# Optimization experiments

Measured on AMD Instinct MI355X. Metric: run time of the kernel, lower is better.

The kernel has to match this reference:

```python
import jax, jax.numpy as jnp
import numpy as np

N = 32; D = 1152; HEADS = 16; HD = D // HEADS; DEPTH = 12
C = 4; GS = 16; P = GS * GS; PL = 16; FE = 256; NC = 1000; MLPD = 4 * D
L = C + P; SCALE = HD ** -0.5


def _ln(x, g, b):
    m = x.mean(-1, keepdims=True)
    v = ((x - m) ** 2).mean(-1, keepdims=True)
    return (x - m) * jax.lax.rsqrt(v + 1e-5) * g + b


def _sincos_pos_embed(dim, gs):
    def _1d(ed, pos):
        omega = 1.0 / 10000 ** (np.arange(ed // 2, dtype=np.float64) / (ed / 2.0))
        out = np.einsum('m,d->md', pos.reshape(-1), omega)
        return np.concatenate([np.sin(out), np.cos(out)], axis=1)
    gw, gh = np.meshgrid(np.arange(gs, dtype=np.float32), np.arange(gs, dtype=np.float32))
    return np.concatenate([_1d(dim // 2, gw), _1d(dim // 2, gh)], axis=1)


def setup_inputs():
    key = jax.random.key(0)
    ks = iter(jax.random.split(key, 64))
    r = lambda *s: 0.02 * jax.random.normal(next(ks), s, dtype=jnp.float32)
    inp = {}
    inp['x'] = jax.random.normal(next(ks), (N, P, PL), dtype=jnp.float32)
    inp['t'] = jax.random.uniform(next(ks), (N,), dtype=jnp.float32) * 1000.0
    inp['y'] = jax.random.randint(next(ks), (N,), 0, NC)
    inp['xw'] = r(PL, D); inp['xb'] = r(D)
    inp['tw1'] = r(FE, D); inp['tb1'] = r(D)
    inp['tw2'] = r(D, D); inp['tb2'] = r(D)
    inp['ytab'] = r(NC + 1, D * C)
    inp['pos'] = jnp.asarray(_sincos_pos_embed(D, GS)[None], dtype=jnp.float32)
    inp['cpos'] = r(1, C, D)
    inp['ln1g'] = 1.0 + r(DEPTH, D); inp['ln1b'] = r(DEPTH, D)
    inp['qkvw'] = r(DEPTH, D, 3 * D)
    inp['qng'] = 1.0 + r(DEPTH, HD); inp['qnb'] = r(DEPTH, HD)
    inp['kng'] = 1.0 + r(DEPTH, HD); inp['knb'] = r(DEPTH, HD)
    inp['pw'] = r(DEPTH, D, D); inp['pb'] = r(DEPTH, D)
    inp['ln2g'] = 1.0 + r(DEPTH, D); inp['ln2b'] = r(DEPTH, D)
    inp['f1w'] = r(DEPTH, D, MLPD); inp['f1b'] = r(DEPTH, MLPD)
    inp['f2w'] = r(DEPTH, MLPD, D); inp['f2b'] = r(DEPTH, D)
    inp['fng'] = 1.0 + r(D); inp['fnb'] = r(D)
    inp['ow'] = r(D, PL); inp['ob'] = r(PL)
    return inp


def reference(x, t, y, xw, xb, tw1, tb1, tw2, tb2, ytab, pos, cpos,
              ln1g, ln1b, qkvw, qng, qnb, kng, knb, pw, pb,
              ln2g, ln2b, f1w, f1b, f2w, f2b, fng, fnb, ow, ob):
    n = x.shape[0]
    # timestep embedding (sinusoidal -> MLP with SiLU)
    half = FE // 2
    freqs = jnp.exp(-jnp.log(jnp.float32(10000.0)) * jnp.arange(half, dtype=jnp.float32) / half)
    a = t[:, None] * freqs[None]
    temb = jnp.concatenate([jnp.cos(a), jnp.sin(a)], axis=-1)  # [N, FE]
    temb = jax.nn.silu(temb @ tw1 + tb1) @ tw2 + tb2           # [N, D]
    # label embedding -> num_cond_tokens conditioning tokens (eval: no label drop)
    cond = ytab[y].reshape(n, C, D) + cpos + temb[:, None, :]  # [N, C, D]
    # patch token projection + fixed sincos pos embed
    xt = x @ xw + xb + pos                                     # [N, P, D]
    tok = jnp.concatenate([cond, xt], axis=1)                  # [N, L, D]
    mask = jnp.triu(jnp.ones((L, L), dtype=bool), k=1)         # causal (True = masked)

    def block(tok, p):
        g1, b1, qw, qg, qb, kg, kb, pww, pbb, g2, b2, w1, bb1, w2, bb2 = p
        h = _ln(tok, g1, b1)
        qkv = (h @ qw).reshape(n, L, 3, HEADS, HD).transpose(2, 0, 3, 1, 4)
        q, k, v = qkv[0], qkv[1], qkv[2]                       # [N, H, L, HD]
        q = _ln(q, qg, qb) * SCALE
        k = _ln(k, kg, kb)
        att = jnp.einsum('nhqd,nhkd->nhqk', q, k)
        att = jnp.where(mask, jnp.float32(-1e9), att)
        att = jax.nn.softmax(att, axis=-1)
        o = jnp.einsum('nhqk,nhkd->nhqd', att, v).transpose(0, 2, 1, 3).reshape(n, L, D)
        tok = tok + (o @ pww + pbb)
        h2 = _ln(tok, g2, b2)
        tok = tok + (jax.nn.gelu(h2 @ w1 + bb1, approximate=True) @ w2 + bb2)
        return tok, None

    tok, _ = jax.lax.scan(block, tok,
                          (ln1g, ln1b, qkvw, qng, qnb, kng, knb, pw, pb,
                           ln2g, ln2b, f1w, f1b, f2w, f2b))
    out = _ln(tok, fng, fnb) @ ow + ob                          # [N, L, PL]
    return out[:, C:]                                           # predictions for patch tokens
```

## Files before the change

kernel.cpp:

```cpp
#include <hip/hip_runtime.h>
#include <hip/hip_bf16.h>
#include <cstdint>

#define DEV __device__ __forceinline__

typedef __attribute__((ext_vector_type(8))) short bf16x8;
typedef __attribute__((ext_vector_type(4))) float f32x4;
typedef unsigned short u16;
typedef unsigned int u32;

constexpr int BN_   = 32;
constexpr int PP    = 256;
constexpr int PL_   = 16;
constexpr int CT    = 4;
constexpr int LL    = 260;
constexpr int DD    = 1152;
constexpr int HH    = 16;
constexpr int HDIM  = 72;
constexpr int DEPTH_= 12;
constexpr int TD    = 3456;
constexpr int MLPD_ = 4608;
constexpr int MREAL = BN_*LL;
constexpr int MPAD  = 8448;
constexpr int LP    = 288;
constexpr int HDP   = 96;
constexpr int HDV   = 80;
constexpr float SCALE_ = 0.11785113019775793f;

constexpr size_t OP_ = (size_t)TD*DD;
constexpr size_t OF1 = OP_ + (size_t)DD*DD;
constexpr size_t OF2 = OF1 + (size_t)MLPD_*DD;
constexpr size_t ARENA_ELEMS = OF2 + (size_t)1280*MLPD_;

DEV u16 f2bf(float f){
    union{float f; u32 i;} c; c.f = f;
    u32 u = c.i;
    u32 r = (u + 0x7fffu + ((u>>16)&1u)) >> 16;
    return (u16)r;
}
DEV float bf2f(u32 u){ union{u32 i; float f;} c; c.i = u<<16; return c.f; }

DEV float wave_sum64(float v){
    #pragma unroll
    for (int off=32; off; off>>=1) v += __shfl_xor(v, off);
    return v;
}
DEV float group16_sum(float v){
    #pragma unroll
    for (int off=8; off; off>>=1) v += __shfl_xor(v, off);
    return v;
}
DEV float gelu_f(float x){
    float u = 0.7978845608028654f * (x + 0.044715f * x*x*x);
    return x / (1.f + __expf(-2.f * u));
}

__global__ void temb1_kernel(const float* __restrict__ t, const float* __restrict__ tw1,
                             const float* __restrict__ tb1, float* __restrict__ e1)
{
    int n = blockIdx.y, j = blockIdx.x*128 + threadIdx.x;
    float tv = t[n];
    float acc = tb1[j];
    const float k = 0.07195578415606394f;
    for (int i = 0; i < 128; ++i) {
        float f = __expf(-k * (float)i);
        float a = tv * f;
        float sa = sinf(a), ca = cosf(a);
        acc += ca * tw1[(size_t)i*DD + j] + sa * tw1[(size_t)(i+128)*DD + j];
    }
    e1[(size_t)n*DD + j] = acc / (1.f + __expf(-acc));
}

__global__ void temb2_kernel(const float* __restrict__ e1, const float* __restrict__ tw2,
                             const float* __restrict__ tb2, float* __restrict__ te)
{
    int n = blockIdx.y, j = blockIdx.x*128 + threadIdx.x;
    float acc = tb2[j];
    const float* er = e1 + (size_t)n*DD;
    for (int kk = 0; kk < DD; ++kk)
        acc += er[kk] * tw2[(size_t)kk*DD + j];
    te[(size_t)n*DD + j] = acc;
}

__global__ void assemble_kernel(const float* __restrict__ x, const int* __restrict__ y,
                                const float* __restrict__ xw, const float* __restrict__ xb,
                                const float* __restrict__ ytab, const float* __restrict__ pos,
                                const float* __restrict__ cpos, const float* __restrict__ te,
                                float* __restrict__ tokf)
{
    int m = blockIdx.x;
    if (m >= MREAL) {
        for (int d = threadIdx.x; d < DD; d += 256) tokf[(size_t)m*DD + d] = 0.f;
        return;
    }
    int n = m / LL, l = m % LL;
    if (l < CT) {
        int cls = y[n];
        const float* yt = ytab + (size_t)cls*(CT*DD) + (size_t)l*DD;
        const float* cp = cpos + (size_t)l*DD;
        const float* tm = te + (size_t)n*DD;
        for (int d = threadIdx.x; d < DD; d += 256)
            tokf[(size_t)m*DD + d] = yt[d] + cp[d] + tm[d];
    } else {
        int p = l - CT;
        const float* xr = x + (size_t)(n*PP + p)*PL_;
        float xv[16];
        #pragma unroll
        for (int i=0;i<16;i++) xv[i] = xr[i];
        const float* pr = pos + (size_t)p*DD;
        for (int d = threadIdx.x; d < DD; d += 256) {
            float acc = xb[d] + pr[d];
            #pragma unroll
            for (int i=0;i<16;i++) acc += xv[i] * xw[(size_t)i*DD + d];
            tokf[(size_t)m*DD + d] = acc;
        }
    }
}

__global__ void convT4_kernel(const float* __restrict__ qkvw, const float* __restrict__ pw,
                              const float* __restrict__ f1w, const float* __restrict__ f2w,
                              u16* __restrict__ arena)
{
    __shared__ float tile[64][65];
    int id = blockIdx.x;
    const float* W; u16* WT; int K, Nw, t0;
    if (id < 972)        { W = qkvw; WT = arena;        K = DD;    Nw = TD;    t0 = id; }
    else if (id < 1296)  { W = pw;   WT = arena + OP_;  K = DD;    Nw = DD;    t0 = id - 972; }
    else if (id < 2592)  { W = f1w;  WT = arena + OF1;  K = DD;    Nw = MLPD_; t0 = id - 1296; }
    else                 { W = f2w;  WT = arena + OF2;  K = MLPD_; Nw = DD;    t0 = id - 2592; }
    int nx = Nw >> 6;
    int nb = (t0 % nx) * 64, kb = (t0 / nx) * 64;
    int tx = threadIdx.x & 63, ty = threadIdx.x >> 6;
    #pragma unroll
    for (int r=0;r<16;r++)
        tile[r*4 + ty][tx] = W[(size_t)(kb + r*4 + ty)*Nw + nb + tx];
    __syncthreads();
    int j = threadIdx.x & 63, i2 = threadIdx.x >> 6;
    #pragma unroll
    for (int r=0;r<16;r++) {
        int n = i2 + r*4;
        WT[(size_t)(nb + n)*K + kb + j] = f2bf(tile[j][n]);
    }
}

__global__ void ln_kernel(const float* __restrict__ src, const float* __restrict__ g,
                          const float* __restrict__ b, u16* __restrict__ dst)
{
    int lane = threadIdx.x & 63, w = threadIdx.x >> 6;
    int m = blockIdx.x*4 + w;
    const float* row = src + (size_t)m * DD;
    float4 v[5];
    float s = 0.f, ss = 0.f;
    #pragma unroll
    for (int i=0;i<5;i++) {
        int idx = i*64 + lane;
        if (idx < 288) {
            v[i] = ((const float4*)row)[idx];
            s  += v[i].x + v[i].y + v[i].z + v[i].w;
            ss += v[i].x*v[i].x + v[i].y*v[i].y + v[i].z*v[i].z + v[i].w*v[i].w;
        }
    }
    s = wave_sum64(s); ss = wave_sum64(ss);
    float mean = s * (1.f/DD);
    float var  = ss * (1.f/DD) - mean*mean;
    float rs   = rsqrtf(var + 1e-5f);
    u16* orow = dst + (size_t)m*DD;
    #pragma unroll
    for (int i=0;i<5;i++) {
        int idx = i*64 + lane;
        if (idx < 288) {
            int c0 = idx*4;
            float4 gg = ((const float4*)g)[idx];
            float4 bb = ((const float4*)b)[idx];
            ushort4 o;
            o.x = f2bf((v[i].x-mean)*rs*gg.x + bb.x);
            o.y = f2bf((v[i].y-mean)*rs*gg.y + bb.y);
            o.z = f2bf((v[i].z-mean)*rs*gg.z + bb.z);
            o.w = f2bf((v[i].w-mean)*rs*gg.w + bb.w);
            *(ushort4*)(orow + c0) = o;
        }
    }
}

template<int EPI>
__global__ __launch_bounds__(256, 4)
void gemm97_kernel(const u16* __restrict__ A, const u16* __restrict__ BT,
                   int K, int Nreal, u16* __restrict__ outb, float* __restrict__ outf,
                   const float* __restrict__ bias)
{
    __shared__ u16 As[128][64];
    __shared__ u16 Bs[128][64];
    const int tid = threadIdx.x;
    const int lane = tid & 63, wv = tid >> 6;
    const int wq = wv >> 1, wp = wv & 1;
    const int l15 = lane & 15, g4 = lane >> 4;

    const int id = blockIdx.x + gridDim.x * blockIdx.y;
    const int total = gridDim.x * gridDim.y;
    const int qch = total >> 3, rch = total & 7;
    const int xcd = id & 7, ps = id >> 3;
    const int wg = (xcd < rch ? xcd*(qch+1) : rch*(qch+1) + (xcd-rch)*qch) + ps;
    const int m0 = (wg / gridDim.x) * 128, n0 = (wg % gridDim.x) * 128;

    const int rr = tid >> 3, chv = tid & 7;
    const int cxo = (chv ^ (rr & 7)) * 8;
    const u16* gA = A  + (size_t)(m0 + rr) * K + cxo;
    const u16* gB = BT + (size_t)(n0 + rr) * K + cxo;

    auto stageA = [&](int kk) {
        #pragma unroll
        for (int i=0;i<4;i++)
            __builtin_amdgcn_global_load_lds(
                (const __attribute__((address_space(1))) void*)(gA + (size_t)(i*32)*K + kk),
                (__attribute__((address_space(3))) void*)(&As[i*32 + wv*8][0]), 16, 0, 0);
    };
    auto stageB = [&](int kk) {
        #pragma unroll
        for (int i=0;i<4;i++)
            __builtin_amdgcn_global_load_lds(
                (const __attribute__((address_space(1))) void*)(gB + (size_t)(i*32)*K + kk),
                (__attribute__((address_space(3))) void*)(&Bs[i*32 + wv*8][0]), 16, 0, 0);
    };
    auto rdA = [&](int m, int ks)->bf16x8 {
        int r = wq*64 + m*16 + l15;
        return *(const bf16x8*)(&As[r][((ks*4 + g4) ^ (r & 7))*8]);
    };
    auto rdB = [&](int n, int ks)->bf16x8 {
        int r = wp*64 + n*16 + l15;
        return *(const bf16x8*)(&Bs[r][((ks*4 + g4) ^ (r & 7))*8]);
    };

    f32x4 acc[4][4];
    #pragma unroll
    for (int i=0;i<4;i++)
        #pragma unroll
        for (int j=0;j<4;j++) acc[i][j] = (f32x4){0.f,0.f,0.f,0.f};

    const int NT = K >> 6;
    for (int t = 0; t < NT; ++t) {
        stageA(t << 6); stageB(t << 6);
        __syncthreads();
        #pragma unroll
        for (int ks=0; ks<2; ++ks) {
            bf16x8 aF[4], bF[4];
            #pragma unroll
            for (int m=0;m<4;m++) aF[m] = rdA(m, ks);
            #pragma unroll
            for (int n=0;n<4;n++) bF[n] = rdB(n, ks);
            #pragma unroll
            for (int m=0;m<4;m++)
                #pragma unroll
                for (int n=0;n<4;n++)
                    acc[m][n] = __builtin_amdgcn_mfma_f32_16x16x32_bf16(aF[m], bF[n], acc[m][n], 0,0,0);
        }
        __syncthreads();
    }

    #pragma unroll
    for (int m=0;m<4;m++) {
        const int gr = m0 + wq*64 + m*16 + g4*4;
        #pragma unroll
        for (int n=0;n<4;n++) {
            const int gc = n0 + wp*64 + n*16 + l15;
            if (gc < Nreal) {
                #pragma unroll
                for (int r=0;r<4;r++) {
                    float vv = acc[m][n][r];
                    size_t oi = (size_t)(gr + r)*Nreal + gc;
                    if constexpr (EPI == 0) {
                        outb[oi] = f2bf(vv);
                    } else if constexpr (EPI == 1) {
                        outb[oi] = f2bf(gelu_f(vv + bias[gc]));
                    } else {
                        outf[oi] = outf[oi] + vv + bias[gc];
                    }
                }
            }
        }
    }
}

__global__ void qknorm_kernel(const u16* __restrict__ qkv,
                              const float* __restrict__ qg, const float* __restrict__ qb,
                              const float* __restrict__ kg, const float* __restrict__ kb,
                              u16* __restrict__ qn, u16* __restrict__ kn)
{
    int lane = threadIdx.x & 63, w = threadIdx.x >> 6;
    int s = lane & 15, g = lane >> 4;
    int idx = blockIdx.x*16 + w*4 + g;
    int l = idx % LP; int nh = idx / LP;
    int h = nh & 15, n = nh >> 4;
    u32* qrow = (u32*)(qn + (size_t)idx * HDP);
    u32* krow = (u32*)(kn + (size_t)idx * HDP);
    if (l >= LL) {
        #pragma unroll
        for (int j=0;j<3;j++) { qrow[s + 16*j] = 0u; krow[s + 16*j] = 0u; }
        return;
    }
    size_t m = (size_t)n*LL + l;
    const u32* qs = (const u32*)(qkv + m*TD + h*HDIM);
    const u32* ks = (const u32*)(qkv + m*TD + DD + h*HDIM);

    float q0[3], q1[3], k0[3], k1[3];
    float sq = 0.f, sqq = 0.f, sk = 0.f, skk = 0.f;
    #pragma unroll
    for (int j=0;j<3;j++) {
        int c = s + 16*j;
        q0[j]=q1[j]=k0[j]=k1[j]=0.f;
        if (c < 36) {
            u32 uq = qs[c]; q0[j] = bf2f(uq & 0xffffu); q1[j] = bf2f(uq >> 16);
            u32 uk = ks[c]; k0[j] = bf2f(uk & 0xffffu); k1[j] = bf2f(uk >> 16);
        }
        sq += q0[j]+q1[j]; sqq += q0[j]*q0[j]+q1[j]*q1[j];
        sk += k0[j]+k1[j]; skk += k0[j]*k0[j]+k1[j]*k1[j];
    }
    sq = group16_sum(sq); sqq = group16_sum(sqq);
    sk = group16_sum(sk); skk = group16_sum(skk);
    float mq = sq*(1.f/HDIM), vq = sqq*(1.f/HDIM) - mq*mq, rq = rsqrtf(vq + 1e-5f);
    float mk = sk*(1.f/HDIM), vk = skk*(1.f/HDIM) - mk*mk, rk = rsqrtf(vk + 1e-5f);
    #pragma unroll
    for (int j=0;j<3;j++) {
        int c = s + 16*j;
        if (c < 36) {
            float o0 = ((q0[j]-mq)*rq*qg[c*2]   + qb[c*2]  ) * SCALE_;
            float o1 = ((q1[j]-mq)*rq*qg[c*2+1] + qb[c*2+1]) * SCALE_;
            qrow[c] = (u32)f2bf(o0) | ((u32)f2bf(o1) << 16);
            float p0 = (k0[j]-mk)*rk*kg[c*2]   + kb[c*2];
            float p1 = (k1[j]-mk)*rk*kg[c*2+1] + kb[c*2+1];
            krow[c] = (u32)f2bf(p0) | ((u32)f2bf(p1) << 16);
        } else {
            qrow[c] = 0u; krow[c] = 0u;
        }
    }
}

__global__ void vtran_kernel(const u16* __restrict__ qkv, u16* __restrict__ vt)
{
    __shared__ u16 tile[32][81];
    int b = blockIdx.x; int h = b & 15, n = b >> 4;
    int tid = threadIdx.x;
    const size_t vbase = 2*DD + (size_t)h*HDIM;
    u16* vto = vt + (size_t)b * (HDV*LP);
    for (int lt = 0; lt < 9; ++lt) {
        #pragma unroll
        for (int e = 0; e < 9; ++e) {
            int ei = e*256 + tid;
            int r = ei / 72, c = ei - r*72;
            int l = lt*32 + r;
            u16 v = 0;
            if (l < LL) v = qkv[((size_t)n*LL + l)*TD + vbase + c];
            tile[r][c] = v;
        }
        __syncthreads();
        int j = tid & 31, hd0 = tid >> 5;
        #pragma unroll
        for (int e = 0; e < 10; ++e) {
            int hd = hd0 + e*8;
            u16 v = (hd < HDIM) ? tile[j][hd] : (u16)0;
            vto[(size_t)hd*LP + lt*32 + j] = v;
        }
        __syncthreads();
    }
}

__global__ __launch_bounds__(256)
void attn_kernel(const u16* __restrict__ qn, const u16* __restrict__ kn,
                 const u16* __restrict__ vt, u16* __restrict__ obuf)
{
    __shared__ u16 Pl[4][512];
    int b = blockIdx.x; int h = b & 15, n = b >> 4;
    int by = blockIdx.y;
    int lane = threadIdx.x & 63, w = threadIdx.x >> 6;
    const u16* qb_ = qn + (size_t)b * (LP*HDP);
    const u16* kb_ = kn + (size_t)b * (LP*HDP);
    const u16* vb_ = vt + (size_t)b * (HDV*LP);
    const int l15 = lane & 15, g4 = lane >> 4;
    const int slot = w + 4*by;

    for (int t = slot; t < 17; t += 8) {
        int qr0 = t*16;
        bf16x8 aq[3];
        #pragma unroll
        for (int fi=0; fi<3; ++fi)
            aq[fi] = *(const bf16x8*)(qb_ + (size_t)(qr0 + l15)*HDP + fi*32 + g4*8);
        f32x4 o[5];
        #pragma unroll
        for (int ht=0; ht<5; ++ht) o[ht] = (f32x4){0.f,0.f,0.f,0.f};
        float mrow[4], ssum[4];
        #pragma unroll
        for (int r=0;r<4;r++){ mrow[r] = -1e30f; ssum[r] = 0.f; }

        int umax = (qr0 + 15) >> 5;
        for (int u = 0; u <= umax; ++u) {
            f32x4 sacc[2];
            #pragma unroll
            for (int cc=0; cc<2; ++cc) {
                sacc[cc] = (f32x4){0.f,0.f,0.f,0.f};
                #pragma unroll
                for (int fi=0; fi<3; ++fi) {
                    bf16x8 bk = *(const bf16x8*)(kb_ + (size_t)(u*32 + cc*16 + l15)*HDP + fi*32 + g4*8);
                    sacc[cc] = __builtin_amdgcn_mfma_f32_16x16x32_bf16(aq[fi], bk, sacc[cc], 0,0,0);
                }
            }
            float pv0[4], pv1[4];
            #pragma unroll
            for (int r=0;r<4;r++) {
                int qi = qr0 + g4*4 + r;
                float s0 = ((u*32 + l15)      <= qi) ? sacc[0][r] : -1e30f;
                float s1 = ((u*32 + 16 + l15) <= qi) ? sacc[1][r] : -1e30f;
                float mx = fmaxf(s0, s1);
                mx = fmaxf(mx, __shfl_xor(mx, 1));
                mx = fmaxf(mx, __shfl_xor(mx, 2));
                mx = fmaxf(mx, __shfl_xor(mx, 4));
                mx = fmaxf(mx, __shfl_xor(mx, 8));
                float nm = fmaxf(mrow[r], mx);
                float sc = __expf(mrow[r] - nm);
                float p0 = __expf(s0 - nm), p1 = __expf(s1 - nm);
                float rsm = p0 + p1;
                rsm += __shfl_xor(rsm, 1); rsm += __shfl_xor(rsm, 2);
                rsm += __shfl_xor(rsm, 4); rsm += __shfl_xor(rsm, 8);
                ssum[r] = ssum[r]*sc + rsm;
                mrow[r] = nm;
                #pragma unroll
                for (int ht=0; ht<5; ++ht) o[ht][r] *= sc;
                pv0[r] = p0; pv1[r] = p1;
            }
            u16* pw_ = Pl[w];
            #pragma unroll
            for (int r=0;r<4;r++) {
                pw_[(g4*4+r)*32 + l15]      = f2bf(pv0[r]);
                pw_[(g4*4+r)*32 + 16 + l15] = f2bf(pv1[r]);
            }
            bf16x8 aP = *(const bf16x8*)(pw_ + l15*32 + g4*8);
            #pragma unroll
            for (int ht=0; ht<5; ++ht) {
                bf16x8 bv = *(const bf16x8*)(vb_ + (size_t)(ht*16 + l15)*LP + u*32 + g4*8);
                o[ht] = __builtin_amdgcn_mfma_f32_16x16x32_bf16(aP, bv, o[ht], 0,0,0);
            }
        }
        #pragma unroll
        for (int r=0;r<4;r++) {
            int l = qr0 + g4*4 + r;
            if (l < LL) {
                float inv = 1.f / ssum[r];
                size_t mro = ((size_t)n*LL + l)*DD + (size_t)h*HDIM;
                #pragma unroll
                for (int ht=0; ht<5; ++ht) {
                    int hd = ht*16 + l15;
                    if (hd < HDIM) obuf[mro + hd] = f2bf(o[ht][r] * inv);
                }
            }
        }
    }
}

__global__ __launch_bounds__(256)
void outproj_kernel(const float* __restrict__ tokf, const float* __restrict__ g,
                    const float* __restrict__ b, const float* __restrict__ ow,
                    const float* __restrict__ ob, float* __restrict__ out)
{
    __shared__ float hrow[4][1152];
    int lane = threadIdx.x & 63, w = threadIdx.x >> 6;
    int idx = blockIdx.x*4 + w;
    int n = idx >> 8, p = idx & 255;
    size_t m = (size_t)n*LL + CT + p;
    const float* row = tokf + m*DD;
    float4 v[5];
    float s = 0.f, ss = 0.f;
    #pragma unroll
    for (int i=0;i<5;i++) {
        int id = i*64 + lane;
        if (id < 288) {
            v[i] = ((const float4*)row)[id];
            s  += v[i].x + v[i].y + v[i].z + v[i].w;
            ss += v[i].x*v[i].x + v[i].y*v[i].y + v[i].z*v[i].z + v[i].w*v[i].w;
        }
    }
    s = wave_sum64(s); ss = wave_sum64(ss);
    float mean = s*(1.f/DD), var = ss*(1.f/DD) - mean*mean;
    float rs = rsqrtf(var + 1e-5f);
    #pragma unroll
    for (int i=0;i<5;i++) {
        int id = i*64 + lane;
        if (id < 288) {
            int c0 = id*4;
            float4 gg = ((const float4*)g)[id];
            float4 bb = ((const float4*)b)[id];
            hrow[w][c0+0] = (v[i].x-mean)*rs*gg.x + bb.x;
            hrow[w][c0+1] = (v[i].y-mean)*rs*gg.y + bb.y;
            hrow[w][c0+2] = (v[i].z-mean)*rs*gg.z + bb.z;
            hrow[w][c0+3] = (v[i].w-mean)*rs*gg.w + bb.w;
        }
    }
    __syncthreads();
    int c = lane & 15, q = lane >> 4;
    float acc = 0.f;
    const float* hq = hrow[w] + q*288;
    const float* owq = ow + (size_t)(q*288)*16 + c;
    #pragma unroll 4
    for (int d = 0; d < 288; ++d)
        acc += hq[d] * owq[(size_t)d*16];
    acc += __shfl_xor(acc, 16);
    acc += __shfl_xor(acc, 32);
    if (lane < 16) {
        out[((size_t)n*PP + p)*PL_ + c] = acc + ob[c];
    }
}

extern "C" void kernel_launch(void* const* d_in, const int* in_sizes, int n_in,
                              void* d_out, int out_size, void* d_ws, size_t ws_size,
                              hipStream_t stream)
{
    const float* x    = (const float*)d_in[0];
    const float* t    = (const float*)d_in[1];
    const int*   y    = (const int*)d_in[2];
    const float* xw   = (const float*)d_in[3];
    const float* xb   = (const float*)d_in[4];
    const float* tw1  = (const float*)d_in[5];
    const float* tb1  = (const float*)d_in[6];
    const float* tw2  = (const float*)d_in[7];
    const float* tb2  = (const float*)d_in[8];
    const float* ytab = (const float*)d_in[9];
    const float* pos  = (const float*)d_in[10];
    const float* cpos = (const float*)d_in[11];
    const float* ln1g = (const float*)d_in[12];
    const float* ln1b = (const float*)d_in[13];
    const float* qkvw = (const float*)d_in[14];
    const float* qng  = (const float*)d_in[15];
    const float* qnbi = (const float*)d_in[16];
    const float* kng  = (const float*)d_in[17];
    const float* knbi = (const float*)d_in[18];
    const float* pw   = (const float*)d_in[19];
    const float* pb   = (const float*)d_in[20];
    const float* ln2g = (const float*)d_in[21];
    const float* ln2b = (const float*)d_in[22];
    const float* f1w  = (const float*)d_in[23];
    const float* f1b  = (const float*)d_in[24];
    const float* f2w  = (const float*)d_in[25];
    const float* f2b  = (const float*)d_in[26];
    const float* fng  = (const float*)d_in[27];
    const float* fnb  = (const float*)d_in[28];
    const float* ow   = (const float*)d_in[29];
    const float* ob   = (const float*)d_in[30];
    float* out = (float*)d_out;

    char* wsb = (char*)d_ws;
    size_t off = 0;
    auto alloc = [&](size_t bytes)->void* {
        void* p = wsb + off; off += (bytes + 255) & ~(size_t)255; return p;
    };
    float* tokf = (float*)alloc((size_t)MPAD*DD*4);
    u16*   hbuf = (u16*)  alloc((size_t)MPAD*DD*2);
    u16*   qkvb = (u16*)  alloc((size_t)MPAD*TD*2);
    u16*   qnb_ = (u16*)  alloc((size_t)BN_*HH*LP*HDP*2);
    u16*   knb_ = (u16*)  alloc((size_t)BN_*HH*LP*HDP*2);
    u16*   vtb  = (u16*)  alloc((size_t)BN_*HH*HDV*LP*2);
    u16*   obuf = (u16*)  alloc((size_t)MPAD*DD*2);
    u16*   mid  = (u16*)  alloc((size_t)MPAD*MLPD_*2);
    u16*   wT   = (u16*)  alloc(ARENA_ELEMS*2);
    float* e1   = (float*)alloc((size_t)BN_*DD*4);
    float* te   = (float*)alloc((size_t)BN_*DD*4);
    (void)ws_size; (void)in_sizes; (void)n_in; (void)out_size;

    temb1_kernel<<<dim3(9,32),128,0,stream>>>(t, tw1, tb1, e1);
    temb2_kernel<<<dim3(9,32),128,0,stream>>>(e1, tw2, tb2, te);
    assemble_kernel<<<MPAD,256,0,stream>>>(x, y, xw, xb, ytab, pos, cpos, te, tokf);

    for (int L_ = 0; L_ < DEPTH_; ++L_) {
        convT4_kernel<<<3888,256,0,stream>>>(qkvw + (size_t)L_*DD*TD, pw + (size_t)L_*DD*DD,
                                             f1w + (size_t)L_*DD*MLPD_, f2w + (size_t)L_*MLPD_*DD, wT);
        ln_kernel<<<MPAD/4,256,0,stream>>>(tokf, ln1g + L_*DD, ln1b + L_*DD, hbuf);
        gemm97_kernel<0><<<dim3(27, 66),256,0,stream>>>(hbuf, wT, DD, TD, qkvb, nullptr, nullptr);
        qknorm_kernel<<<BN_*HH*LP/16,256,0,stream>>>(qkvb, qng + L_*HDIM, qnbi + L_*HDIM,
                                                     kng + L_*HDIM, knbi + L_*HDIM, qnb_, knb_);
        vtran_kernel<<<BN_*HH,256,0,stream>>>(qkvb, vtb);
        attn_kernel<<<dim3(BN_*HH, 2),256,0,stream>>>(qnb_, knb_, vtb, obuf);
        gemm97_kernel<2><<<dim3(9, 66),256,0,stream>>>(obuf, wT + OP_, DD, DD, nullptr, tokf, pb + L_*DD);
        ln_kernel<<<MPAD/4,256,0,stream>>>(tokf, ln2g + L_*DD, ln2b + L_*DD, hbuf);
        gemm97_kernel<1><<<dim3(36, 66),256,0,stream>>>(hbuf, wT + OF1, DD, MLPD_, mid, nullptr, f1b + L_*MLPD_);
        gemm97_kernel<2><<<dim3(9, 66),256,0,stream>>>(mid, wT + OF2, MLPD_, DD, nullptr, tokf, f2b + L_*DD);
    }
    outproj_kernel<<<(BN_*PP)/4,256,0,stream>>>(tokf, fng, fnb, ow, ob, out);
}
```

Baseline: 5.946 ms.

## Add 256x128-tile 512-thread GEMM for QKV and FC1 projections

```diff
diff --git a/kernel.cpp b/kernel.cpp
--- a/kernel.cpp
+++ b/kernel.cpp
@@ -273,6 +273,102 @@
                         outb[oi] = f2bf(gelu_f(vv + bias[gc]));
                     } else {
                         outf[oi] = outf[oi] + vv + bias[gc];
+                    }
+                }
+            }
+        }
+    }
+}
+
+template<int EPI>
+__global__ __launch_bounds__(512, 4)
+void gemm256_kernel(const u16* __restrict__ A, const u16* __restrict__ BT,
+                    int K, int Nreal, u16* __restrict__ outb,
+                    const float* __restrict__ bias)
+{
+    __shared__ u16 As[256][64];
+    __shared__ u16 Bs[128][64];
+    const int tid = threadIdx.x;
+    const int lane = tid & 63, wv = tid >> 6;
+    const int wm = wv & 3, wn = wv >> 2;
+    const int l15 = lane & 15, g4 = lane >> 4;
+
+    const int id = blockIdx.x + gridDim.x * blockIdx.y;
+    const int total = gridDim.x * gridDim.y;
+    const int qch = total >> 3, rch = total & 7;
+    const int xcd = id & 7, ps = id >> 3;
+    const int wg = (xcd < rch ? xcd*(qch+1) : rch*(qch+1) + (xcd-rch)*qch) + ps;
+    const int m0 = (wg / gridDim.x) * 256, n0 = (wg % gridDim.x) * 128;
+
+    const int rr = tid >> 3, chv = tid & 7;
+    const int cxo = (chv ^ (rr & 7)) * 8;
+    const u16* gA = A  + (size_t)(m0 + rr) * K + cxo;
+    const u16* gB = BT + (size_t)(n0 + rr) * K + cxo;
+
+    auto stageA = [&](int kk) {
+        #pragma unroll
+        for (int i=0;i<4;i++)
+            __builtin_amdgcn_global_load_lds(
+                (const __attribute__((address_space(1))) void*)(gA + (size_t)(i*64)*K + kk),
+                (__attribute__((address_space(3))) void*)(&As[i*64 + wv*8][0]), 16, 0, 0);
+    };
+    auto stageB = [&](int kk) {
+        #pragma unroll
+        for (int i=0;i<2;i++)
+            __builtin_amdgcn_global_load_lds(
+                (const __attribute__((address_space(1))) void*)(gB + (size_t)(i*64)*K + kk),
+                (__attribute__((address_space(3))) void*)(&Bs[i*64 + wv*8][0]), 16, 0, 0);
+    };
+    auto rdA = [&](int m, int ks)->bf16x8 {
+        int r = wm*64 + m*16 + l15;
+        return *(const bf16x8*)(&As[r][((ks*4 + g4) ^ (r & 7))*8]);
+    };
+    auto rdB = [&](int n, int ks)->bf16x8 {
+        int r = wn*64 + n*16 + l15;
+        return *(const bf16x8*)(&Bs[r][((ks*4 + g4) ^ (r & 7))*8]);
+    };
+
+    f32x4 acc[4][4];
+    #pragma unroll
+    for (int i=0;i<4;i++)
+        #pragma unroll
+        for (int j=0;j<4;j++) acc[i][j] = (f32x4){0.f,0.f,0.f,0.f};
+
+    const int NT = K >> 6;
+    for (int t = 0; t < NT; ++t) {
+        stageA(t << 6); stageB(t << 6);
+        __syncthreads();
+        #pragma unroll
+        for (int ks=0; ks<2; ++ks) {
+            bf16x8 aF[4], bF[4];
+            #pragma unroll
+            for (int m=0;m<4;m++) aF[m] = rdA(m, ks);
+            #pragma unroll
+            for (int n=0;n<4;n++) bF[n] = rdB(n, ks);
+            #pragma unroll
+            for (int m=0;m<4;m++)
+                #pragma unroll
+                for (int n=0;n<4;n++)
+                    acc[m][n] = __builtin_amdgcn_mfma_f32_16x16x32_bf16(aF[m], bF[n], acc[m][n], 0,0,0);
+        }
+        __syncthreads();
+    }
+
+    #pragma unroll
+    for (int m=0;m<4;m++) {
+        const int gr = m0 + wm*64 + m*16 + g4*4;
+        #pragma unroll
+        for (int n=0;n<4;n++) {
+            const int gc = n0 + wn*64 + n*16 + l15;
+            if (gc < Nreal) {
+                #pragma unroll
+                for (int r=0;r<4;r++) {
+                    float vv = acc[m][n][r];
+                    size_t oi = (size_t)(gr + r)*Nreal + gc;
+                    if constexpr (EPI == 0) {
+                        outb[oi] = f2bf(vv);
+                    } else {
+                        outb[oi] = f2bf(gelu_f(vv + bias[gc]));
                     }
                 }
             }
@@ -570,14 +666,14 @@
         convT4_kernel<<<3888,256,0,stream>>>(qkvw + (size_t)L_*DD*TD, pw + (size_t)L_*DD*DD,
                                              f1w + (size_t)L_*DD*MLPD_, f2w + (size_t)L_*MLPD_*DD, wT);
         ln_kernel<<<MPAD/4,256,0,stream>>>(tokf, ln1g + L_*DD, ln1b + L_*DD, hbuf);
-        gemm97_kernel<0><<<dim3(27, 66),256,0,stream>>>(hbuf, wT, DD, TD, qkvb, nullptr, nullptr);
+        gemm256_kernel<0><<<dim3(27, 33),512,0,stream>>>(hbuf, wT, DD, TD, qkvb, nullptr);
         qknorm_kernel<<<BN_*HH*LP/16,256,0,stream>>>(qkvb, qng + L_*HDIM, qnbi + L_*HDIM,
                                                      kng + L_*HDIM, knbi + L_*HDIM, qnb_, knb_);
         vtran_kernel<<<BN_*HH,256,0,stream>>>(qkvb, vtb);
         attn_kernel<<<dim3(BN_*HH, 2),256,0,stream>>>(qnb_, knb_, vtb, obuf);
         gemm97_kernel<2><<<dim3(9, 66),256,0,stream>>>(obuf, wT + OP_, DD, DD, nullptr, tokf, pb + L_*DD);
         ln_kernel<<<MPAD/4,256,0,stream>>>(tokf, ln2g + L_*DD, ln2b + L_*DD, hbuf);
-        gemm97_kernel<1><<<dim3(36, 66),256,0,stream>>>(hbuf, wT + OF1, DD, MLPD_, mid, nullptr, f1b + L_*MLPD_);
+        gemm256_kernel<1><<<dim3(36, 33),512,0,stream>>>(hbuf, wT + OF1, DD, MLPD_, mid, f1b + L_*MLPD_);
         gemm97_kernel<2><<<dim3(9, 66),256,0,stream>>>(mid, wT + OF2, MLPD_, DD, nullptr, tokf, f2b + L_*DD);
     }
     outproj_kernel<<<(BN_*PP)/4,256,0,stream>>>(tokf, fng, fnb, ow, ob, out);
```

Result: faster. 5.808 ms (-2.3%).
